# Optimization experiments

Hardware: AMD Instinct MI355X
Metric: run time of the kernel (lower is better)

The kernel has to match this reference:

```python
import jax, jax.numpy as jnp
import numpy as np

D_MODEL = 1024
NHEAD = 16
D_HEAD = D_MODEL // NHEAD


def setup_inputs() -> dict:
    key = jax.random.key(0)
    ks = jax.random.split(key, 11)
    B, S = 4, 1024
    s = 1.0 / np.sqrt(D_MODEL)
    inp = {
        'q_in': jax.random.normal(ks[0], (B, S, D_MODEL), jnp.float32),
        'k_in': jax.random.normal(ks[1], (B, S, D_MODEL), jnp.float32),
        'v_in': jax.random.normal(ks[2], (B, S, D_MODEL), jnp.float32),
        'Wq': jax.random.normal(ks[3], (D_MODEL, D_MODEL), jnp.float32) * s,
        'bq': jnp.zeros((D_MODEL,), jnp.float32),
        'Wk': jax.random.normal(ks[4], (D_MODEL, D_MODEL), jnp.float32) * s,
        'bk': jnp.zeros((D_MODEL,), jnp.float32),
        'Wv': jax.random.normal(ks[5], (D_MODEL, D_MODEL), jnp.float32) * s,
        'bv': jnp.zeros((D_MODEL,), jnp.float32),
        'Wo': jax.random.normal(ks[6], (D_MODEL, D_MODEL), jnp.float32) * s,
        'bo': jnp.zeros((D_MODEL,), jnp.float32),
    }
    return inp


def reference(q_in, k_in, v_in, Wq, bq, Wk, bk, Wv, bv, Wo, bo):
    B, Sq, _ = q_in.shape
    Sk = k_in.shape[1]
    # Linear projections (torch Linear: x @ W.T + b; here W stored as [in, out])
    Q = q_in @ Wq + bq
    K = k_in @ Wk + bk
    V = v_in @ Wv + bv
    # [B, H, S, Dh]
    Qh = Q.reshape(B, Sq, NHEAD, D_HEAD).transpose(0, 2, 1, 3)
    Kh = K.reshape(B, Sk, NHEAD, D_HEAD).transpose(0, 2, 1, 3)
    Vh = V.reshape(B, Sk, NHEAD, D_HEAD).transpose(0, 2, 1, 3)
    scores = jnp.einsum('bhqd,bhkd->bhqk', Qh, Kh) / jnp.sqrt(jnp.float32(D_HEAD))
    attn_weights = jax.nn.softmax(scores, axis=-1)
    attn = jnp.einsum('bhqk,bhkd->bhqd', attn_weights, Vh)
    attn = attn.transpose(0, 2, 1, 3).reshape(B, Sq, D_MODEL)
    out = attn @ Wo + bo
    return out
```

## Files before the change

### kernel.cpp

```cpp
#include <hip/hip_runtime.h>
#include <hip/hip_bf16.h>
#include <cstdint>
#include <cstddef>

typedef __bf16 bf16_t;
typedef __bf16 bf16x8 __attribute__((ext_vector_type(8)));
typedef __bf16 bf16x4 __attribute__((ext_vector_type(4)));
typedef float f32x4 __attribute__((ext_vector_type(4)));

#define DM 1024
#define NHEAD 16
#define DHEAD 64

#define QSCALE 0.18033688011112042f
#define PSHIFT 4.0f
#define RS 72

#define WAITVM(N) asm volatile("s_waitcnt vmcnt(" #N ")" ::: "memory")
#define LGKM0()   asm volatile("s_waitcnt lgkmcnt(0)" ::: "memory")
#define BAR()     do { asm volatile("" ::: "memory"); __builtin_amdgcn_s_barrier(); \
                       asm volatile("" ::: "memory"); } while (0)

__device__ __forceinline__ void gload_lds16(const void* g, void* l) {
    __builtin_amdgcn_global_load_lds(
        (const __attribute__((address_space(1))) void*)g,
        (__attribute__((address_space(3))) void*)l,
        16, 0, 0);
}

__device__ __forceinline__ uint4 cvt8(float4 lo, float4 hi) {
    union { bf16_t b[8]; uint4 u; } o;
    o.b[0] = (bf16_t)lo.x; o.b[1] = (bf16_t)lo.y; o.b[2] = (bf16_t)lo.z; o.b[3] = (bf16_t)lo.w;
    o.b[4] = (bf16_t)hi.x; o.b[5] = (bf16_t)hi.y; o.b[6] = (bf16_t)hi.z; o.b[7] = (bf16_t)hi.w;
    return o.u;
}

__global__ void prep(
    const float* __restrict__ q_in, const float* __restrict__ k_in, const float* __restrict__ v_in,
    bf16_t* __restrict__ Xq, bf16_t* __restrict__ Xk, bf16_t* __restrict__ Xv,
    const float* __restrict__ w0, const float* __restrict__ w1,
    const float* __restrict__ w2, const float* __restrict__ w3,
    bf16_t* __restrict__ t0, bf16_t* __restrict__ t1,
    bf16_t* __restrict__ t2, bf16_t* __restrict__ t3)
{
    __shared__ float tile[64][65];
    int id = blockIdx.x;
    if (id < 6144) {
        int plane = id >> 11;
        int blk = id & 2047;
        const float* x = plane == 0 ? q_in : plane == 1 ? k_in : v_in;
        bf16_t* y      = plane == 0 ? Xq   : plane == 1 ? Xk   : Xv;
        int i = (blk * 256 + threadIdx.x) * 8;
        float4 lo = *(const float4*)&x[i];
        float4 hi = *(const float4*)&x[i + 4];
        *(uint4*)&y[i] = cvt8(lo, hi);
    } else {
        int t = id - 6144;
        int zi = t >> 8;
        int blk = t & 255;
        const float* w = zi == 0 ? w0 : zi == 1 ? w1 : zi == 2 ? w2 : w3;
        bf16_t* wt     = zi == 0 ? t0 : zi == 1 ? t1 : zi == 2 ? t2 : t3;
        int bx = (blk & 15) * 64;
        int by = (blk >> 4) * 64;
        int tx = threadIdx.x & 63, ty = threadIdx.x >> 6;
        for (int j = 0; j < 64; j += 4)
            tile[ty + j][tx] = w[(size_t)(by + ty + j) * DM + bx + tx];
        __syncthreads();
        int nl = threadIdx.x >> 3;
        int kl = (threadIdx.x & 7) * 8;
        for (int j = 0; j < 64; j += 32) {
            int n = nl + j;
            union { bf16_t b[8]; uint4 u; } o;
            for (int i = 0; i < 8; i++)
                o.b[i] = (bf16_t)tile[kl + i][n];
            *(uint4*)&wt[(size_t)(bx + n) * DM + by + kl] = o.u;
        }
    }
}

template <int MODE>
__device__ __forceinline__ void gemm_body(
    const bf16_t* __restrict__ A, const bf16_t* __restrict__ Bt,
    const float* __restrict__ bias, float scale,
    bf16_t* __restrict__ Cb,
    int r0, int c0, bf16_t* AsP, bf16_t* BsP)
{
    const int K = 1024;
    int tid  = threadIdx.x;
    int wave = tid >> 6;
    int lane = tid & 63;
    int quad = lane >> 4;
    int ln   = lane & 15;
    int wr   = wave >> 1;
    int wc   = wave & 1;

    f32x4 acc[4][4];
    for (int rb = 0; rb < 4; rb++)
        for (int cb = 0; cb < 4; cb++)
            acc[rb][cb] = (f32x4){0.f, 0.f, 0.f, 0.f};

    int sr = tid >> 2;
    int sk = (((tid & 3) ^ ((tid >> 3) & 3))) * 8;

    const bf16_t* gA0 = &A[(size_t)(r0 + sr) * K + sk];
    const bf16_t* gA1 = gA0 + (size_t)64 * K;
    const bf16_t* gB0 = &Bt[(size_t)(c0 + sr) * K + sk];
    const bf16_t* gB1 = gB0 + (size_t)64 * K;
    char* lA = (char*)AsP + wave * 1024;
    char* lB = (char*)BsP + wave * 1024;

    int ch = (quad ^ ((ln >> 1) & 3)) * 8;

    auto STAGE = [&](int s, int slot) {
        int k = s * 32;
        int off = slot * 8192;
        gload_lds16(gA0 + k, lA + off);
        gload_lds16(gA1 + k, lA + off + 4096);
        gload_lds16(gB0 + k, lB + off);
        gload_lds16(gB1 + k, lB + off + 4096);
    };
    auto COMPUTE = [&](int slot) {
        const bf16_t* Ab = AsP + slot * 4096;
        const bf16_t* Bb = BsP + slot * 4096;
        bf16x8 af[4], bfv[4];
        #pragma unroll
        for (int rb = 0; rb < 4; rb++)
            af[rb] = *(const bf16x8*)&Ab[(wr * 64 + rb * 16 + ln) * 32 + ch];
        #pragma unroll
        for (int cb = 0; cb < 4; cb++)
            bfv[cb] = *(const bf16x8*)&Bb[(wc * 64 + cb * 16 + ln) * 32 + ch];
        __builtin_amdgcn_s_setprio(1);
        #pragma unroll
        for (int rb = 0; rb < 4; rb++)
            #pragma unroll
            for (int cb = 0; cb < 4; cb++)
                acc[rb][cb] = __builtin_amdgcn_mfma_f32_16x16x32_bf16(af[rb], bfv[cb], acc[rb][cb], 0, 0, 0);
        __builtin_amdgcn_s_setprio(0);
    };

    STAGE(0, 0); STAGE(1, 1);
    WAITVM(4);
    BAR();

    for (int tt = 0; tt < 30; tt += 3) {
        STAGE(tt + 2, 2); COMPUTE(0); WAITVM(4); BAR();
        STAGE(tt + 3, 0); COMPUTE(1); WAITVM(4); BAR();
        STAGE(tt + 4, 1); COMPUTE(2); WAITVM(4); BAR();
    }
    COMPUTE(0); WAITVM(0); BAR();
    COMPUTE(1);

    for (int rb = 0; rb < 4; rb++) {
        for (int cb = 0; cb < 4; cb++) {
            int C = c0 + wc * 64 + cb * 16 + ln;
            for (int r = 0; r < 4; r++) {
                int R = r0 + wr * 64 + rb * 16 + quad * 4 + r;
                float v = acc[rb][cb][r];
                if (MODE == 1) {
                    int b = R >> 10, s = R & 1023;
                    int h = C >> 6,  d = C & 63;
                    Cb[(((size_t)b * NHEAD + h) * 1024 + s) * DHEAD + d] =
                        (bf16_t)((v + bias[C]) * scale);
                } else {
                    Cb[((size_t)(C >> 10) * 1024 + R) * 1024 + (C & 1023)] =
                        (bf16_t)(v + bias[R]);
                }
            }
        }
    }
}

__global__ __launch_bounds__(256, 3) void gemm_qkv(
    const bf16_t* __restrict__ Xq, const bf16_t* __restrict__ Xk, const bf16_t* __restrict__ Xv,
    const bf16_t* __restrict__ Wtq, const bf16_t* __restrict__ Wtk, const bf16_t* __restrict__ Wtv,
    const float* __restrict__ bq, const float* __restrict__ bk, const float* __restrict__ bv,
    bf16_t* __restrict__ Qd, bf16_t* __restrict__ Kd, bf16_t* __restrict__ Vt)
{
    __shared__ __align__(16) bf16_t As[3 * 128 * 32];
    __shared__ __align__(16) bf16_t Bs[3 * 128 * 32];
    int z = blockIdx.z;
    if (z == 0) {
        gemm_body<1>(Xq, Wtq, bq, QSCALE, Qd,
                     blockIdx.x * 128, blockIdx.y * 128, As, Bs);
    } else if (z == 1) {
        gemm_body<1>(Xk, Wtk, bk, 1.0f, Kd,
                     blockIdx.x * 128, blockIdx.y * 128, As, Bs);
    } else {
        gemm_body<2>(Wtv, Xv, bv, 1.0f, Vt,
                     blockIdx.y * 128, blockIdx.x * 128, As, Bs);
    }
}

__global__ __launch_bounds__(256, 2) void gemm_out(
    const bf16_t* __restrict__ At, const bf16_t* __restrict__ Wto,
    const float* __restrict__ bo, float* __restrict__ out)
{
    const int K = 1024;
    __shared__ __align__(16) bf16_t As[3 * 64 * 32];
    __shared__ __align__(16) bf16_t Bs[3 * 128 * 32];

    int tid  = threadIdx.x;
    int wave = tid >> 6;
    int lane = tid & 63;
    int quad = lane >> 4;
    int ln   = lane & 15;

    int r0 = blockIdx.x * 64;
    int c0 = blockIdx.y * 128;

    f32x4 acc[4][2];
    for (int rb = 0; rb < 4; rb++)
        for (int cb = 0; cb < 2; cb++)
            acc[rb][cb] = (f32x4){0.f, 0.f, 0.f, 0.f};

    int sr = tid >> 2;
    int sk = (((tid & 3) ^ ((tid >> 3) & 3))) * 8;

    const bf16_t* gA0 = At  + (size_t)(r0 + sr) * K + sk;
    const bf16_t* gB0 = Wto + (size_t)(c0 + sr) * K + sk;
    const bf16_t* gB1 = gB0 + (size_t)64 * K;
    char* lA = (char*)As + wave * 1024;
    char* lB = (char*)Bs + wave * 1024;

    int ch = (quad ^ ((ln >> 1) & 3)) * 8;

    auto STAGE = [&](int s, int slot) {
        int k = s * 32;
        gload_lds16(gA0 + k, lA + slot * 4096);
        gload_lds16(gB0 + k, lB + slot * 8192);
        gload_lds16(gB1 + k, lB + slot * 8192 + 4096);
    };
    auto COMPUTE = [&](int slot) {
        const bf16_t* Ab = As + slot * 2048;
        const bf16_t* Bb = Bs + slot * 4096;
        bf16x8 af[4], bfv[2];
        #pragma unroll
        for (int rb = 0; rb < 4; rb++)
            af[rb] = *(const bf16x8*)&Ab[(rb * 16 + ln) * 32 + ch];
        #pragma unroll
        for (int cb = 0; cb < 2; cb++)
            bfv[cb] = *(const bf16x8*)&Bb[(wave * 32 + cb * 16 + ln) * 32 + ch];
        __builtin_amdgcn_s_setprio(1);
        #pragma unroll
        for (int rb = 0; rb < 4; rb++)
            #pragma unroll
            for (int cb = 0; cb < 2; cb++)
                acc[rb][cb] = __builtin_amdgcn_mfma_f32_16x16x32_bf16(af[rb], bfv[cb], acc[rb][cb], 0, 0, 0);
        __builtin_amdgcn_s_setprio(0);
    };

    STAGE(0, 0); STAGE(1, 1);
    WAITVM(3);
    BAR();

    for (int tt = 0; tt < 30; tt += 3) {
        STAGE(tt + 2, 2); COMPUTE(0); WAITVM(3); BAR();
        STAGE(tt + 3, 0); COMPUTE(1); WAITVM(3); BAR();
        STAGE(tt + 4, 1); COMPUTE(2); WAITVM(3); BAR();
    }
    COMPUTE(0); WAITVM(0); BAR();
    COMPUTE(1);

    for (int rb = 0; rb < 4; rb++) {
        for (int cb = 0; cb < 2; cb++) {
            int C = c0 + wave * 32 + cb * 16 + ln;
            float bn = bo[C];
            for (int r = 0; r < 4; r++) {
                int R = r0 + rb * 16 + quad * 4 + r;
                out[(size_t)R * DM + C] = acc[rb][cb][r] + bn;
            }
        }
    }
}

__global__ __launch_bounds__(256) void attn7(
    const bf16_t* __restrict__ Q,
    const bf16_t* __restrict__ K,
    const bf16_t* __restrict__ Vt,
    bf16_t* __restrict__ O)
{
    __shared__ __align__(16) bf16_t Ks[2][64 * RS];
    __shared__ __align__(16) bf16_t Vs[2][64 * RS];
    __shared__ __align__(16) bf16_t Ps[4][32 * RS];

    int tid  = threadIdx.x;
    int wave = tid >> 6;
    int lane = tid & 63;
    int quad = lane >> 4;
    int ln   = lane & 15;

    int bh = blockIdx.x;
    int q0w = blockIdx.y * 128 + wave * 32;

    const bf16_t* Qb = Q  + (size_t)bh * 65536;
    const bf16_t* Kb = K  + (size_t)bh * 65536;
    const bf16_t* Vb = Vt + (size_t)bh * 65536;

    int srow = tid >> 3;
    int scol = (tid & 7) * 8;
    const bf16_t* gK0 = Kb + (size_t)srow * 64 + scol;
    const bf16_t* gK1 = gK0 + 32 * 64;
    const bf16_t* gV0 = Vb + (size_t)srow * 1024 + scol;
    const bf16_t* gV1 = gV0 + 32 * 1024;

    bf16x8 aq0[2], aq1[2];
    for (int h = 0; h < 2; h++) {
        aq0[h] = *(const bf16x8*)&Qb[(size_t)(q0w + h * 16 + ln) * 64 + quad * 8];
        aq1[h] = *(const bf16x8*)&Qb[(size_t)(q0w + h * 16 + ln) * 64 + 32 + quad * 8];
    }

    uint4 rK0 = *(const uint4*)gK0;
    uint4 rK1 = *(const uint4*)gK1;
    uint4 rV0 = *(const uint4*)gV0;
    uint4 rV1 = *(const uint4*)gV1;
    *(uint4*)&Ks[0][srow * RS + scol]        = rK0;
    *(uint4*)&Ks[0][(32 + srow) * RS + scol] = rK1;
    *(uint4*)&Vs[0][srow * RS + scol]        = rV0;
    *(uint4*)&Vs[0][(32 + srow) * RS + scol] = rV1;
    gK0 += 4096; gK1 += 4096; gV0 += 64; gV1 += 64;
    rK0 = *(const uint4*)gK0;
    rK1 = *(const uint4*)gK1;
    rV0 = *(const uint4*)gV0;
    rV1 = *(const uint4*)gV1;

    float l_lane[2] = {0.f, 0.f};
    f32x4 o_acc[2][4];
    for (int h = 0; h < 2; h++)
        for (int cb = 0; cb < 4; cb++)
            o_acc[h][cb] = (f32x4){0.f, 0.f, 0.f, 0.f};

    bf16_t* Pw = Ps[wave];

    LGKM0();
    BAR();

    for (int kt = 0; kt < 16; kt++) {
        const bf16_t* Kc = Ks[kt & 1];
        const bf16_t* Vc = Vs[kt & 1];
        bf16_t* Kn = Ks[(kt + 1) & 1];
        bf16_t* Vn = Vs[(kt + 1) & 1];

        if (kt < 15) {
            *(uint4*)&Kn[srow * RS + scol]        = rK0;
            *(uint4*)&Kn[(32 + srow) * RS + scol] = rK1;
            *(uint4*)&Vn[srow * RS + scol]        = rV0;
            *(uint4*)&Vn[(32 + srow) * RS + scol] = rV1;
        }
        if (kt < 14) {
            gK0 += 4096; gK1 += 4096; gV0 += 64; gV1 += 64;
            rK0 = *(const uint4*)gK0;
            rK1 = *(const uint4*)gK1;
            rV0 = *(const uint4*)gV0;
            rV1 = *(const uint4*)gV1;
        }

        f32x4 sc[4][2];
        for (int kb = 0; kb < 4; kb++) {
            bf16x8 kf0 = *(const bf16x8*)&Kc[(kb * 16 + ln) * RS + quad * 8];
            bf16x8 kf1 = *(const bf16x8*)&Kc[(kb * 16 + ln) * RS + 32 + quad * 8];
            for (int h = 0; h < 2; h++) {
                f32x4 a = (f32x4){0.f, 0.f, 0.f, 0.f};
                a = __builtin_amdgcn_mfma_f32_16x16x32_bf16(kf0, aq0[h], a, 0, 0, 0);
                a = __builtin_amdgcn_mfma_f32_16x16x32_bf16(kf1, aq1[h], a, 0, 0, 0);
                sc[kb][h] = a;
            }
        }

        for (int kb = 0; kb < 4; kb++) {
            for (int h = 0; h < 2; h++) {
                float p0 = __builtin_amdgcn_exp2f(sc[kb][h][0] - PSHIFT);
                float p1 = __builtin_amdgcn_exp2f(sc[kb][h][1] - PSHIFT);
                float p2 = __builtin_amdgcn_exp2f(sc[kb][h][2] - PSHIFT);
                float p3 = __builtin_amdgcn_exp2f(sc[kb][h][3] - PSHIFT);
                l_lane[h] += (p0 + p1) + (p2 + p3);
                bf16x4 pk = (bf16x4){(bf16_t)p0, (bf16_t)p1, (bf16_t)p2, (bf16_t)p3};
                *(bf16x4*)&Pw[(h * 16 + ln) * RS + kb * 16 + quad * 4] = pk;
            }
        }

        for (int kc = 0; kc < 2; kc++) {
            bf16x8 ap0 = *(const bf16x8*)&Pw[ln * RS + kc * 32 + quad * 8];
            bf16x8 ap1 = *(const bf16x8*)&Pw[(16 + ln) * RS + kc * 32 + quad * 8];
            for (int cb = 0; cb < 4; cb++) {
                bf16x8 vf = *(const bf16x8*)&Vc[(cb * 16 + ln) * RS + kc * 32 + quad * 8];
                o_acc[0][cb] = __builtin_amdgcn_mfma_f32_16x16x32_bf16(ap0, vf, o_acc[0][cb], 0, 0, 0);
                o_acc[1][cb] = __builtin_amdgcn_mfma_f32_16x16x32_bf16(ap1, vf, o_acc[1][cb], 0, 0, 0);
            }
        }

        if (kt < 15) {
            LGKM0();
            BAR();
        }
    }

    int b = bh >> 4, hd = bh & 15;
    for (int h = 0; h < 2; h++) {
        float l = l_lane[h];
        l += __shfl_xor(l, 16);
        l += __shfl_xor(l, 32);
        float invq[4];
        for (int r = 0; r < 4; r++)
            invq[r] = 1.f / __shfl(l, quad * 4 + r);
        for (int cb = 0; cb < 4; cb++) {
            for (int r = 0; r < 4; r++) {
                int q = q0w + h * 16 + quad * 4 + r;
                int d = cb * 16 + ln;
                O[((size_t)b * 1024 + q) * DM + hd * 64 + d] = (bf16_t)(o_acc[h][cb][r] * invq[r]);
            }
        }
    }
}

extern "C" void kernel_launch(void* const* d_in, const int* in_sizes, int n_in,
                              void* d_out, int out_size, void* d_ws, size_t ws_size,
                              hipStream_t stream) {
    const float* q_in = (const float*)d_in[0];
    const float* k_in = (const float*)d_in[1];
    const float* v_in = (const float*)d_in[2];
    const float* Wq   = (const float*)d_in[3];
    const float* bq   = (const float*)d_in[4];
    const float* Wk   = (const float*)d_in[5];
    const float* bk   = (const float*)d_in[6];
    const float* Wv   = (const float*)d_in[7];
    const float* bv   = (const float*)d_in[8];
    const float* Wo   = (const float*)d_in[9];
    const float* bo   = (const float*)d_in[10];

    char* ws = (char*)d_ws;
    const size_t MB = 1024ull * 1024ull;
    bf16_t* Xq  = (bf16_t*)(ws);
    bf16_t* Xk  = (bf16_t*)(ws + 8 * MB);
    bf16_t* Xv  = (bf16_t*)(ws + 16 * MB);
    bf16_t* Wtq = (bf16_t*)(ws + 24 * MB);
    bf16_t* Wtk = (bf16_t*)(ws + 26 * MB);
    bf16_t* Wtv = (bf16_t*)(ws + 28 * MB);
    bf16_t* Wto = (bf16_t*)(ws + 30 * MB);
    bf16_t* Qd  = (bf16_t*)(ws + 32 * MB);
    bf16_t* Kd  = (bf16_t*)(ws + 40 * MB);
    bf16_t* Vt  = (bf16_t*)(ws + 48 * MB);
    bf16_t* At  = Xq;

    prep<<<7168, 256, 0, stream>>>(q_in, k_in, v_in, Xq, Xk, Xv,
                                   Wq, Wk, Wv, Wo, Wtq, Wtk, Wtv, Wto);

    gemm_qkv<<<dim3(32, 8, 3), 256, 0, stream>>>(Xq, Xk, Xv,
                                                 Wtq, Wtk, Wtv, bq, bk, bv, Qd, Kd, Vt);

    attn7<<<dim3(64, 8), 256, 0, stream>>>(Qd, Kd, Vt, At);

    gemm_out<<<dim3(64, 8), 256, 0, stream>>>(At, Wto, bo, (float*)d_out);
}
```

Before: 200.7 us.

## Fuse fp32-to-bf16 activation conversion into QKV GEMM operand staging

Removes the separate activation conversion pass from the prep kernel. The QKV GEMM now loads fp32 activations through registers, converts them with packed bf16 conversion instructions, and writes them to LDS, while the weight operand still uses direct global-to-LDS loads. This avoids writing and re-reading the 24MB bf16 activation copies. In exchange, the GEMM reads twice the bytes for activations, and each of the 8 column blocks re-reads the same fp32 rows. It also adds register pressure and VALU work in the main loop.

```diff
diff --git a/kernel.cpp b/kernel.cpp
--- a/kernel.cpp
+++ b/kernel.cpp
@@ -20,6 +20,7 @@
 #define LGKM0()   asm volatile("s_waitcnt lgkmcnt(0)" ::: "memory")
 #define BAR()     do { asm volatile("" ::: "memory"); __builtin_amdgcn_s_barrier(); \
                        asm volatile("" ::: "memory"); } while (0)
+#define CVTPK(d, a, b) asm("v_cvt_pk_bf16_f32 %0, %1, %2" : "=v"(d) : "v"(a), "v"(b))
 
 __device__ __forceinline__ void gload_lds16(const void* g, void* l) {
     __builtin_amdgcn_global_load_lds(
@@ -28,16 +29,7 @@
         16, 0, 0);
 }
 
-__device__ __forceinline__ uint4 cvt8(float4 lo, float4 hi) {
-    union { bf16_t b[8]; uint4 u; } o;
-    o.b[0] = (bf16_t)lo.x; o.b[1] = (bf16_t)lo.y; o.b[2] = (bf16_t)lo.z; o.b[3] = (bf16_t)lo.w;
-    o.b[4] = (bf16_t)hi.x; o.b[5] = (bf16_t)hi.y; o.b[6] = (bf16_t)hi.z; o.b[7] = (bf16_t)hi.w;
-    return o.u;
-}
-
 __global__ void prep(
-    const float* __restrict__ q_in, const float* __restrict__ k_in, const float* __restrict__ v_in,
-    bf16_t* __restrict__ Xq, bf16_t* __restrict__ Xk, bf16_t* __restrict__ Xv,
     const float* __restrict__ w0, const float* __restrict__ w1,
     const float* __restrict__ w2, const float* __restrict__ w3,
     bf16_t* __restrict__ t0, bf16_t* __restrict__ t1,
@@ -45,42 +37,30 @@
 {
     __shared__ float tile[64][65];
     int id = blockIdx.x;
-    if (id < 6144) {
-        int plane = id >> 11;
-        int blk = id & 2047;
-        const float* x = plane == 0 ? q_in : plane == 1 ? k_in : v_in;
-        bf16_t* y      = plane == 0 ? Xq   : plane == 1 ? Xk   : Xv;
-        int i = (blk * 256 + threadIdx.x) * 8;
-        float4 lo = *(const float4*)&x[i];
-        float4 hi = *(const float4*)&x[i + 4];
-        *(uint4*)&y[i] = cvt8(lo, hi);
-    } else {
-        int t = id - 6144;
-        int zi = t >> 8;
-        int blk = t & 255;
-        const float* w = zi == 0 ? w0 : zi == 1 ? w1 : zi == 2 ? w2 : w3;
-        bf16_t* wt     = zi == 0 ? t0 : zi == 1 ? t1 : zi == 2 ? t2 : t3;
-        int bx = (blk & 15) * 64;
-        int by = (blk >> 4) * 64;
-        int tx = threadIdx.x & 63, ty = threadIdx.x >> 6;
-        for (int j = 0; j < 64; j += 4)
-            tile[ty + j][tx] = w[(size_t)(by + ty + j) * DM + bx + tx];
-        __syncthreads();
-        int nl = threadIdx.x >> 3;
-        int kl = (threadIdx.x & 7) * 8;
-        for (int j = 0; j < 64; j += 32) {
-            int n = nl + j;
-            union { bf16_t b[8]; uint4 u; } o;
-            for (int i = 0; i < 8; i++)
-                o.b[i] = (bf16_t)tile[kl + i][n];
-            *(uint4*)&wt[(size_t)(bx + n) * DM + by + kl] = o.u;
-        }
-    }
-}
-
-template <int MODE>
+    int zi = id >> 8;
+    int blk = id & 255;
+    const float* w = zi == 0 ? w0 : zi == 1 ? w1 : zi == 2 ? w2 : w3;
+    bf16_t* wt     = zi == 0 ? t0 : zi == 1 ? t1 : zi == 2 ? t2 : t3;
+    int bx = (blk & 15) * 64;
+    int by = (blk >> 4) * 64;
+    int tx = threadIdx.x & 63, ty = threadIdx.x >> 6;
+    for (int j = 0; j < 64; j += 4)
+        tile[ty + j][tx] = w[(size_t)(by + ty + j) * DM + bx + tx];
+    __syncthreads();
+    int nl = threadIdx.x >> 3;
+    int kl = (threadIdx.x & 7) * 8;
+    for (int j = 0; j < 64; j += 32) {
+        int n = nl + j;
+        union { bf16_t b[8]; uint4 u; } o;
+        for (int i = 0; i < 8; i++)
+            o.b[i] = (bf16_t)tile[kl + i][n];
+        *(uint4*)&wt[(size_t)(bx + n) * DM + by + kl] = o.u;
+    }
+}
+
+template <int MODE, bool AF32>
 __device__ __forceinline__ void gemm_body(
-    const bf16_t* __restrict__ A, const bf16_t* __restrict__ Bt,
+    const void* __restrict__ Aop, const void* __restrict__ Bop,
     const float* __restrict__ bias, float scale,
     bf16_t* __restrict__ Cb,
     int r0, int c0, bf16_t* AsP, bf16_t* BsP)
@@ -99,25 +79,51 @@
         for (int cb = 0; cb < 4; cb++)
             acc[rb][cb] = (f32x4){0.f, 0.f, 0.f, 0.f};
 
-    int sr = tid >> 2;
-    int sk = (((tid & 3) ^ ((tid >> 3) & 3))) * 8;
-
-    const bf16_t* gA0 = &A[(size_t)(r0 + sr) * K + sk];
-    const bf16_t* gA1 = gA0 + (size_t)64 * K;
-    const bf16_t* gB0 = &Bt[(size_t)(c0 + sr) * K + sk];
-    const bf16_t* gB1 = gB0 + (size_t)64 * K;
-    char* lA = (char*)AsP + wave * 1024;
-    char* lB = (char*)BsP + wave * 1024;
+    int sr  = tid >> 2;
+    int sk8 = ((tid & 3) ^ ((tid >> 3) & 3)) * 8;
+
+    const float*  fF;
+    const bf16_t* gG0;
+    char* lF; char* lG;
+    if (AF32) {
+        fF  = (const float*)Aop  + (size_t)(r0 + sr) * K + sk8;
+        gG0 = (const bf16_t*)Bop + (size_t)(c0 + sr) * K + sk8;
+        lF  = (char*)AsP + tid * 16;
+        lG  = (char*)BsP + wave * 1024;
+    } else {
+        fF  = (const float*)Bop  + (size_t)(c0 + sr) * K + sk8;
+        gG0 = (const bf16_t*)Aop + (size_t)(r0 + sr) * K + sk8;
+        lF  = (char*)BsP + tid * 16;
+        lG  = (char*)AsP + wave * 1024;
+    }
+    const float*  fF1 = fF  + (size_t)64 * K;
+    const bf16_t* gG1 = gG0 + (size_t)64 * K;
 
     int ch = (quad ^ ((ln >> 1) & 3)) * 8;
 
-    auto STAGE = [&](int s, int slot) {
-        int k = s * 32;
-        int off = slot * 8192;
-        gload_lds16(gA0 + k, lA + off);
-        gload_lds16(gA1 + k, lA + off + 4096);
-        gload_lds16(gB0 + k, lB + off);
-        gload_lds16(gB1 + k, lB + off + 4096);
+    f32x4 f0_0, f0_1, f0_2, f0_3;
+    f32x4 f1_0, f1_1, f1_2, f1_3;
+
+#define F_ISSUE(S, kk) do { \
+    f##S##_0 = *(const f32x4*)(fF  + (kk)); \
+    f##S##_1 = *(const f32x4*)(fF  + (kk) + 4); \
+    f##S##_2 = *(const f32x4*)(fF1 + (kk)); \
+    f##S##_3 = *(const f32x4*)(fF1 + (kk) + 4); \
+} while (0)
+
+#define F_WRITE(S, SLOT) do { \
+    uint4 w0, w1; \
+    CVTPK(w0.x, f##S##_0.x, f##S##_0.y); CVTPK(w0.y, f##S##_0.z, f##S##_0.w); \
+    CVTPK(w0.z, f##S##_1.x, f##S##_1.y); CVTPK(w0.w, f##S##_1.z, f##S##_1.w); \
+    CVTPK(w1.x, f##S##_2.x, f##S##_2.y); CVTPK(w1.y, f##S##_2.z, f##S##_2.w); \
+    CVTPK(w1.z, f##S##_3.x, f##S##_3.y); CVTPK(w1.w, f##S##_3.z, f##S##_3.w); \
+    *(uint4*)(lF + (SLOT) * 8192)        = w0; \
+    *(uint4*)(lF + (SLOT) * 8192 + 4096) = w1; \
+} while (0)
+
+    auto G_ISSUE = [&](int kk, int slot) {
+        gload_lds16(gG0 + kk, lG + slot * 8192);
+        gload_lds16(gG1 + kk, lG + slot * 8192 + 4096);
     };
     auto COMPUTE = [&](int slot) {
         const bf16_t* Ab = AsP + slot * 4096;
@@ -138,17 +144,37 @@
         __builtin_amdgcn_s_setprio(0);
     };
 
-    STAGE(0, 0); STAGE(1, 1);
-    WAITVM(4);
-    BAR();
-
-    for (int tt = 0; tt < 30; tt += 3) {
-        STAGE(tt + 2, 2); COMPUTE(0); WAITVM(4); BAR();
-        STAGE(tt + 3, 0); COMPUTE(1); WAITVM(4); BAR();
-        STAGE(tt + 4, 1); COMPUTE(2); WAITVM(4); BAR();
-    }
-    COMPUTE(0); WAITVM(0); BAR();
+    G_ISSUE(0, 0);  F_ISSUE(0, 0);
+    G_ISSUE(32, 1); F_ISSUE(1, 32);
+    WAITVM(6);
+    F_WRITE(0, 0);
+    LGKM0(); BAR();
+
+    int kk = 64;
+    for (int t6 = 0; t6 < 5; ++t6) {
+        G_ISSUE(kk, 2); F_ISSUE(0, kk); COMPUTE(0);
+        WAITVM(6); F_WRITE(1, 1); LGKM0(); BAR(); kk += 32;
+
+        G_ISSUE(kk, 0); F_ISSUE(1, kk); COMPUTE(1);
+        WAITVM(6); F_WRITE(0, 2); LGKM0(); BAR(); kk += 32;
+
+        G_ISSUE(kk, 1); F_ISSUE(0, kk); COMPUTE(2);
+        WAITVM(6); F_WRITE(1, 0); LGKM0(); BAR(); kk += 32;
+
+        G_ISSUE(kk, 2); F_ISSUE(1, kk); COMPUTE(0);
+        WAITVM(6); F_WRITE(0, 1); LGKM0(); BAR(); kk += 32;
+
+        G_ISSUE(kk, 0); F_ISSUE(0, kk); COMPUTE(1);
+        WAITVM(6); F_WRITE(1, 2); LGKM0(); BAR(); kk += 32;
+
+        G_ISSUE(kk, 1); F_ISSUE(1, kk); COMPUTE(2);
+        WAITVM(6); F_WRITE(0, 0); LGKM0(); BAR(); kk += 32;
+    }
+    COMPUTE(0); WAITVM(0); F_WRITE(1, 1); LGKM0(); BAR();
     COMPUTE(1);
+
+#undef F_ISSUE
+#undef F_WRITE
 
     for (int rb = 0; rb < 4; rb++) {
         for (int cb = 0; cb < 4; cb++) {
@@ -171,7 +197,7 @@
 }
 
 __global__ __launch_bounds__(256, 3) void gemm_qkv(
-    const bf16_t* __restrict__ Xq, const bf16_t* __restrict__ Xk, const bf16_t* __restrict__ Xv,
+    const float* __restrict__ q_in, const float* __restrict__ k_in, const float* __restrict__ v_in,
     const bf16_t* __restrict__ Wtq, const bf16_t* __restrict__ Wtk, const bf16_t* __restrict__ Wtv,
     const float* __restrict__ bq, const float* __restrict__ bk, const float* __restrict__ bv,
     bf16_t* __restrict__ Qd, bf16_t* __restrict__ Kd, bf16_t* __restrict__ Vt)
@@ -180,14 +206,14 @@
     __shared__ __align__(16) bf16_t Bs[3 * 128 * 32];
     int z = blockIdx.z;
     if (z == 0) {
-        gemm_body<1>(Xq, Wtq, bq, QSCALE, Qd,
-                     blockIdx.x * 128, blockIdx.y * 128, As, Bs);
+        gemm_body<1, true>(q_in, Wtq, bq, QSCALE, Qd,
+                           blockIdx.x * 128, blockIdx.y * 128, As, Bs);
     } else if (z == 1) {
-        gemm_body<1>(Xk, Wtk, bk, 1.0f, Kd,
-                     blockIdx.x * 128, blockIdx.y * 128, As, Bs);
+        gemm_body<1, true>(k_in, Wtk, bk, 1.0f, Kd,
+                           blockIdx.x * 128, blockIdx.y * 128, As, Bs);
     } else {
-        gemm_body<2>(Wtv, Xv, bv, 1.0f, Vt,
-                     blockIdx.y * 128, blockIdx.x * 128, As, Bs);
+        gemm_body<2, false>(Wtv, v_in, bv, 1.0f, Vt,
+                            blockIdx.y * 128, blockIdx.x * 128, As, Bs);
     }
 }
 
@@ -429,9 +455,7 @@
 
     char* ws = (char*)d_ws;
     const size_t MB = 1024ull * 1024ull;
-    bf16_t* Xq  = (bf16_t*)(ws);
-    bf16_t* Xk  = (bf16_t*)(ws + 8 * MB);
-    bf16_t* Xv  = (bf16_t*)(ws + 16 * MB);
+    bf16_t* At  = (bf16_t*)(ws);
     bf16_t* Wtq = (bf16_t*)(ws + 24 * MB);
     bf16_t* Wtk = (bf16_t*)(ws + 26 * MB);
     bf16_t* Wtv = (bf16_t*)(ws + 28 * MB);
@@ -439,12 +463,10 @@
     bf16_t* Qd  = (bf16_t*)(ws + 32 * MB);
     bf16_t* Kd  = (bf16_t*)(ws + 40 * MB);
     bf16_t* Vt  = (bf16_t*)(ws + 48 * MB);
-    bf16_t* At  = Xq;
-
-    prep<<<7168, 256, 0, stream>>>(q_in, k_in, v_in, Xq, Xk, Xv,
-                                   Wq, Wk, Wv, Wo, Wtq, Wtk, Wtv, Wto);
-
-    gemm_qkv<<<dim3(32, 8, 3), 256, 0, stream>>>(Xq, Xk, Xv,
+
+    prep<<<1024, 256, 0, stream>>>(Wq, Wk, Wv, Wo, Wtq, Wtk, Wtv, Wto);
+
+    gemm_qkv<<<dim3(32, 8, 3), 256, 0, stream>>>(q_in, k_in, v_in,
                                                  Wtq, Wtk, Wtv, bq, bk, bv, Qd, Kd, Vt);
 
     attn7<<<dim3(64, 8), 256, 0, stream>>>(Qd, Kd, Vt, At);
```

New measurement: 211.4 us. 5.3% more time.

## Double per-wave query rows in attention to reuse K/V tiles across more queries

Applied to the files above, without the earlier changes.

Each wave now handles 64 query rows instead of 32, so a block covers 256 queries and the grid halves along the query dimension. Each K/V tile staged into shared memory is reused across twice as many query rows, which cuts global K/V traffic and barrier count per query. The softmax exp is also fused directly after each score MFMA instead of going through a separate score array. In exchange the kernel uses more registers and more LDS (the P buffer doubles), and the grid has fewer blocks (256), which may underfill the GPU's compute units.

```diff
diff --git a/kernel.cpp b/kernel.cpp
--- a/kernel.cpp
+++ b/kernel.cpp
@@ -273,7 +273,7 @@
     }
 }
 
-__global__ __launch_bounds__(256) void attn7(
+__global__ __launch_bounds__(256) void attn8(
     const bf16_t* __restrict__ Q,
     const bf16_t* __restrict__ K,
     const bf16_t* __restrict__ Vt,
@@ -281,7 +281,7 @@
 {
     __shared__ __align__(16) bf16_t Ks[2][64 * RS];
     __shared__ __align__(16) bf16_t Vs[2][64 * RS];
-    __shared__ __align__(16) bf16_t Ps[4][32 * RS];
+    __shared__ __align__(16) bf16_t Ps[4][64 * RS];
 
     int tid  = threadIdx.x;
     int wave = tid >> 6;
@@ -290,7 +290,7 @@
     int ln   = lane & 15;
 
     int bh = blockIdx.x;
-    int q0w = blockIdx.y * 128 + wave * 32;
+    int q0w = blockIdx.y * 256 + wave * 64;
 
     const bf16_t* Qb = Q  + (size_t)bh * 65536;
     const bf16_t* Kb = K  + (size_t)bh * 65536;
@@ -303,8 +303,9 @@
     const bf16_t* gV0 = Vb + (size_t)srow * 1024 + scol;
     const bf16_t* gV1 = gV0 + 32 * 1024;
 
-    bf16x8 aq0[2], aq1[2];
-    for (int h = 0; h < 2; h++) {
+    bf16x8 aq0[4], aq1[4];
+    #pragma unroll
+    for (int h = 0; h < 4; h++) {
         aq0[h] = *(const bf16x8*)&Qb[(size_t)(q0w + h * 16 + ln) * 64 + quad * 8];
         aq1[h] = *(const bf16x8*)&Qb[(size_t)(q0w + h * 16 + ln) * 64 + 32 + quad * 8];
     }
@@ -323,9 +324,11 @@
     rV0 = *(const uint4*)gV0;
     rV1 = *(const uint4*)gV1;
 
-    float l_lane[2] = {0.f, 0.f};
-    f32x4 o_acc[2][4];
-    for (int h = 0; h < 2; h++)
+    float l_lane[4] = {0.f, 0.f, 0.f, 0.f};
+    f32x4 o_acc[4][4];
+    #pragma unroll
+    for (int h = 0; h < 4; h++)
+        #pragma unroll
         for (int cb = 0; cb < 4; cb++)
             o_acc[h][cb] = (f32x4){0.f, 0.f, 0.f, 0.f};
 
@@ -354,37 +357,37 @@
             rV1 = *(const uint4*)gV1;
         }
 
-        f32x4 sc[4][2];
+        #pragma unroll
         for (int kb = 0; kb < 4; kb++) {
             bf16x8 kf0 = *(const bf16x8*)&Kc[(kb * 16 + ln) * RS + quad * 8];
             bf16x8 kf1 = *(const bf16x8*)&Kc[(kb * 16 + ln) * RS + 32 + quad * 8];
-            for (int h = 0; h < 2; h++) {
+            #pragma unroll
+            for (int h = 0; h < 4; h++) {
                 f32x4 a = (f32x4){0.f, 0.f, 0.f, 0.f};
                 a = __builtin_amdgcn_mfma_f32_16x16x32_bf16(kf0, aq0[h], a, 0, 0, 0);
                 a = __builtin_amdgcn_mfma_f32_16x16x32_bf16(kf1, aq1[h], a, 0, 0, 0);
-                sc[kb][h] = a;
-            }
-        }
-
-        for (int kb = 0; kb < 4; kb++) {
-            for (int h = 0; h < 2; h++) {
-                float p0 = __builtin_amdgcn_exp2f(sc[kb][h][0] - PSHIFT);
-                float p1 = __builtin_amdgcn_exp2f(sc[kb][h][1] - PSHIFT);
-                float p2 = __builtin_amdgcn_exp2f(sc[kb][h][2] - PSHIFT);
-                float p3 = __builtin_amdgcn_exp2f(sc[kb][h][3] - PSHIFT);
+                float p0 = __builtin_amdgcn_exp2f(a[0] - PSHIFT);
+                float p1 = __builtin_amdgcn_exp2f(a[1] - PSHIFT);
+                float p2 = __builtin_amdgcn_exp2f(a[2] - PSHIFT);
+                float p3 = __builtin_amdgcn_exp2f(a[3] - PSHIFT);
                 l_lane[h] += (p0 + p1) + (p2 + p3);
                 bf16x4 pk = (bf16x4){(bf16_t)p0, (bf16_t)p1, (bf16_t)p2, (bf16_t)p3};
                 *(bf16x4*)&Pw[(h * 16 + ln) * RS + kb * 16 + quad * 4] = pk;
             }
         }
 
+        #pragma unroll
         for (int kc = 0; kc < 2; kc++) {
-            bf16x8 ap0 = *(const bf16x8*)&Pw[ln * RS + kc * 32 + quad * 8];
-            bf16x8 ap1 = *(const bf16x8*)&Pw[(16 + ln) * RS + kc * 32 + quad * 8];
+            bf16x8 ap[4];
+            #pragma unroll
+            for (int h = 0; h < 4; h++)
+                ap[h] = *(const bf16x8*)&Pw[(h * 16 + ln) * RS + kc * 32 + quad * 8];
+            #pragma unroll
             for (int cb = 0; cb < 4; cb++) {
                 bf16x8 vf = *(const bf16x8*)&Vc[(cb * 16 + ln) * RS + kc * 32 + quad * 8];
-                o_acc[0][cb] = __builtin_amdgcn_mfma_f32_16x16x32_bf16(ap0, vf, o_acc[0][cb], 0, 0, 0);
-                o_acc[1][cb] = __builtin_amdgcn_mfma_f32_16x16x32_bf16(ap1, vf, o_acc[1][cb], 0, 0, 0);
+                #pragma unroll
+                for (int h = 0; h < 4; h++)
+                    o_acc[h][cb] = __builtin_amdgcn_mfma_f32_16x16x32_bf16(ap[h], vf, o_acc[h][cb], 0, 0, 0);
             }
         }
 
@@ -395,7 +398,7 @@
     }
 
     int b = bh >> 4, hd = bh & 15;
-    for (int h = 0; h < 2; h++) {
+    for (int h = 0; h < 4; h++) {
         float l = l_lane[h];
         l += __shfl_xor(l, 16);
         l += __shfl_xor(l, 32);
@@ -447,7 +450,7 @@
     gemm_qkv<<<dim3(32, 8, 3), 256, 0, stream>>>(Xq, Xk, Xv,
                                                  Wtq, Wtk, Wtv, bq, bk, bv, Qd, Kd, Vt);
 
-    attn7<<<dim3(64, 8), 256, 0, stream>>>(Qd, Kd, Vt, At);
+    attn8<<<dim3(64, 4), 256, 0, stream>>>(Qd, Kd, Vt, At);
 
     gemm_out<<<dim3(64, 8), 256, 0, stream>>>(At, Wto, bo, (float*)d_out);
 }
```

Result: slower. 204.8 us (+2.0%).
